# Performance work log

Measured on AMD Instinct MI355X. Metric: run time of the kernel, lower is better.

## Reference

```python
import jax, jax.numpy as jnp
import numpy as np

N_NODES = 500_000
HIDDEN = 128
REDUCED = HIDDEN // 2
N_GRAPHS = 4096


def setup_inputs() -> dict:
    key = jax.random.key(0)
    k_x, k_b, k_w1, k_w2 = jax.random.split(key, 4)
    x = jax.random.normal(k_x, (N_NODES, HIDDEN), dtype=jnp.float32)
    batch = jnp.sort(jax.random.randint(k_b, (N_NODES,), 0, N_GRAPHS, dtype=jnp.int64))
    # Xavier-uniform init like the torch module; biases zero.
    lim1 = float(np.sqrt(6.0 / (HIDDEN + REDUCED)))
    lim2 = float(np.sqrt(6.0 / (REDUCED + HIDDEN)))
    W1 = jax.random.uniform(k_w1, (HIDDEN, REDUCED), minval=-lim1, maxval=lim1, dtype=jnp.float32)
    b1 = jnp.zeros((REDUCED,), dtype=jnp.float32)
    W2 = jax.random.uniform(k_w2, (REDUCED, HIDDEN), minval=-lim2, maxval=lim2, dtype=jnp.float32)
    b2 = jnp.zeros((HIDDEN,), dtype=jnp.float32)
    return {"x": x, "batch": batch, "size": N_GRAPHS, "W1": W1, "b1": b1, "W2": W2, "b2": b2}


def reference(x, batch, size, W1, b1, W2, b2):
    # scatter-sum pool over graphs: [G, H]
    pooled = jax.ops.segment_sum(x, batch, num_segments=size)
    # squeeze-excite MLP + sigmoid gate
    h = jax.nn.relu(pooled @ W1 + b1)          # [G, H/2]
    y = jax.nn.sigmoid(h @ W2 + b2)            # [G, H]
    # gather-broadcast gate back to nodes and modulate features
    return x * y[batch]                        # [N, H]
```

## Files before the change

### kernel.cpp

```cpp
#include <hip/hip_runtime.h>

#define HIDDEN  128
#define REDUCED 64
#define NGRAPHS 4096

typedef float f4 __attribute__((ext_vector_type(4)));

__global__ void seg_starts_kernel(const int* __restrict__ batch,
                                  int* __restrict__ starts, int n_nodes) {
    const int g = blockIdx.x * blockDim.x + threadIdx.x;
    if (g >= NGRAPHS) return;
    int lo = 0, hi = n_nodes;
    while (lo < hi) { int mid = (lo + hi) >> 1; if (batch[mid] < g) lo = mid + 1; else hi = mid; }
    starts[g] = lo;
    if (g == 0) starts[NGRAPHS] = n_nodes;
}

__global__ void __launch_bounds__(256, 4)
fused_kernel(const float* __restrict__ x,
             const int* __restrict__ starts,
             const float* __restrict__ W1, const float* __restrict__ b1,
             const float* __restrict__ W2, const float* __restrict__ b2,
             float* __restrict__ out) {
    const int g = blockIdx.x;
    const int t = threadIdx.x;
    const int lo = starts[g], hi = starts[g + 1];
    const int r = t >> 5, c = t & 31;
    const f4* __restrict__ x4 = (const f4*)x;

    f4 acc = {0.f, 0.f, 0.f, 0.f};
    for (int n = lo + r; n < hi; n += 8) {
        acc += x4[(size_t)n * 32 + c];
    }

    __shared__ f4 red[8][32];
    __shared__ float p_s[HIDDEN];
    __shared__ float h_s[REDUCED];
    __shared__ float y_s[HIDDEN];
    red[r][c] = acc;
    __syncthreads();
    if (r == 0) {
        f4 s = red[0][c];
        #pragma unroll
        for (int k = 1; k < 8; ++k) s += red[k][c];
        ((f4*)p_s)[c] = s;
    }
    __syncthreads();

    if (t < REDUCED) {
        float a1 = b1[t];
        #pragma unroll 8
        for (int i = 0; i < HIDDEN; ++i) a1 = fmaf(p_s[i], W1[i * REDUCED + t], a1);
        h_s[t] = a1 > 0.f ? a1 : 0.f;
    }
    __syncthreads();
    if (t < HIDDEN) {
        float a2 = b2[t];
        #pragma unroll 8
        for (int j = 0; j < REDUCED; ++j) a2 = fmaf(h_s[j], W2[j * HIDDEN + t], a2);
        y_s[t] = 1.f / (1.f + __expf(-a2));
    }
    __syncthreads();

    const f4 yv = ((const f4*)y_s)[c];
    f4* __restrict__ out4 = (f4*)out;
    for (int n = lo + r; n < hi; n += 8) {
        const f4 v = __builtin_nontemporal_load(x4 + (size_t)n * 32 + c);
        f4 o;
        o.x = v.x * yv.x; o.y = v.y * yv.y; o.z = v.z * yv.z; o.w = v.w * yv.w;
        __builtin_nontemporal_store(o, out4 + (size_t)n * 32 + c);
    }
}

extern "C" void kernel_launch(void* const* d_in, const int* in_sizes, int n_in,
                              void* d_out, int out_size, void* d_ws, size_t ws_size,
                              hipStream_t stream) {
    const float* x     = (const float*)d_in[0];
    const int*   batch = (const int*)d_in[1];
    const float* W1 = (const float*)d_in[3];
    const float* b1 = (const float*)d_in[4];
    const float* W2 = (const float*)d_in[5];
    const float* b2 = (const float*)d_in[6];
    float* out = (float*)d_out;

    const int n_nodes = in_sizes[0] / HIDDEN;

    int* starts = (int*)d_ws;

    seg_starts_kernel<<<(NGRAPHS + 255) / 256, 256, 0, stream>>>(batch, starts, n_nodes);
    fused_kernel<<<NGRAPHS, 256, 0, stream>>>(x, starts, W1, b1, W2, b2, out);
}
```

Before: 472.5 us.

## Stage segment rows in LDS via direct global-to-LDS loads to avoid second read of x

Result: faster. 462.2 us (-2.2%).

```diff
diff --git a/kernel.cpp b/kernel.cpp
--- a/kernel.cpp
+++ b/kernel.cpp
@@ -3,8 +3,17 @@
 #define HIDDEN  128
 #define REDUCED 64
 #define NGRAPHS 4096
+#define ROWCAP  108
 
 typedef float f4 __attribute__((ext_vector_type(4)));
+
+__device__ __forceinline__ void gload_lds16(const void* gsrc, void* ldst) {
+    auto g = reinterpret_cast<const __attribute__((address_space(1))) unsigned int*>(
+        reinterpret_cast<uintptr_t>(gsrc));
+    auto l = reinterpret_cast<__attribute__((address_space(3))) unsigned int*>(
+        reinterpret_cast<uintptr_t>(ldst));
+    __builtin_amdgcn_global_load_lds(g, l, 16, 0, 0);
+}
 
 __global__ void seg_starts_kernel(const int* __restrict__ batch,
                                   int* __restrict__ starts, int n_nodes) {
@@ -16,7 +25,7 @@
     if (g == 0) starts[NGRAPHS] = n_nodes;
 }
 
-__global__ void __launch_bounds__(256, 4)
+__global__ void __launch_bounds__(256, 2)
 fused_kernel(const float* __restrict__ x,
              const int* __restrict__ starts,
              const float* __restrict__ W1, const float* __restrict__ b1,
@@ -25,18 +34,33 @@
     const int g = blockIdx.x;
     const int t = threadIdx.x;
     const int lo = starts[g], hi = starts[g + 1];
+    const int cnt = hi - lo;
+    const int staged = cnt < ROWCAP ? cnt : ROWCAP;
     const int r = t >> 5, c = t & 31;
-    const f4* __restrict__ x4 = (const f4*)x;
+    const int w = t >> 6;
+    const int half = (t >> 5) & 1;
 
-    f4 acc = {0.f, 0.f, 0.f, 0.f};
-    for (int n = lo + r; n < hi; n += 8) {
-        acc += x4[(size_t)n * 32 + c];
-    }
-
+    __shared__ f4 sbuf[ROWCAP * 32];
     __shared__ f4 red[8][32];
     __shared__ float p_s[HIDDEN];
     __shared__ float h_s[REDUCED];
     __shared__ float y_s[HIDDEN];
+
+    const f4* __restrict__ x4 = (const f4*)x;
+
+    for (int p = w; 2 * p < staged; p += 4) {
+        const int nrel = 2 * p + half;
+        if (nrel < staged)
+            gload_lds16(x4 + (size_t)(lo + nrel) * 32 + c, &sbuf[p * 64]);
+    }
+    asm volatile("s_waitcnt vmcnt(0)" ::: "memory");
+    __syncthreads();
+
+    f4 acc = {0.f, 0.f, 0.f, 0.f};
+    int nrel = r;
+    for (; nrel < staged; nrel += 8) acc += sbuf[nrel * 32 + c];
+    for (; nrel < cnt;    nrel += 8) acc += x4[(size_t)(lo + nrel) * 32 + c];
+
     red[r][c] = acc;
     __syncthreads();
     if (r == 0) {
@@ -64,11 +88,14 @@
 
     const f4 yv = ((const f4*)y_s)[c];
     f4* __restrict__ out4 = (f4*)out;
-    for (int n = lo + r; n < hi; n += 8) {
-        const f4 v = __builtin_nontemporal_load(x4 + (size_t)n * 32 + c);
-        f4 o;
-        o.x = v.x * yv.x; o.y = v.y * yv.y; o.z = v.z * yv.z; o.w = v.w * yv.w;
-        __builtin_nontemporal_store(o, out4 + (size_t)n * 32 + c);
+    nrel = r;
+    for (; nrel < staged; nrel += 8) {
+        const f4 v = sbuf[nrel * 32 + c];
+        __builtin_nontemporal_store(v * yv, out4 + (size_t)(lo + nrel) * 32 + c);
+    }
+    for (; nrel < cnt; nrel += 8) {
+        const f4 v = x4[(size_t)(lo + nrel) * 32 + c];
+        __builtin_nontemporal_store(v * yv, out4 + (size_t)(lo + nrel) * 32 + c);
     }
 }
 
```
